# Optimization experiments

Hardware: AMD Instinct MI355X
Metric: run time of the kernel (lower is better)

## Reference

```python
import jax, jax.numpy as jnp
import numpy as np

N, K, H, HEADS, DE, MULT = 8000, 32, 256, 8, 128, 2
DH = H // HEADS
BIG_NEG = -1e9


def _ln(x, g, b):
    mu = x.mean(-1, keepdims=True)
    var = ((x - mu) ** 2).mean(-1, keepdims=True)
    return (x - mu) * jax.lax.rsqrt(var + 1e-5) * g + b


def setup_inputs() -> dict:
    key = jax.random.key(0)
    ks = iter(jax.random.split(key, 64))
    def w(shape, s=0.05):
        return (jax.random.normal(next(ks), shape, jnp.float32) * s)
    stdv = float(np.sqrt(6.0 / (HEADS + DH)))
    inp = {
        'node_features': jax.random.normal(next(ks), (N, H), jnp.float32),
        'edge_features': jax.random.normal(next(ks), (N, K, H), jnp.float32),
        'edge_attr_raw': jax.random.normal(next(ks), (N, K, DE), jnp.float32),
        'angle_embedding': jax.random.normal(next(ks), (N, HEADS, K, K), jnp.float32) * 0.1,
        'ln1n_g': jnp.ones((H,)), 'ln1n_b': jnp.zeros((H,)),
        'ln1e_g': jnp.ones((H,)), 'ln1e_b': jnp.zeros((H,)),
        'W_ea': w((DE, H)), 'b_ea': jnp.zeros((H,)),
        'W_nh': w((H, H)), 'b_nh': jnp.zeros((H,)),
        'W_eh': w((H, H)), 'b_eh': jnp.zeros((H,)),
        'W_gate': w((2 * H, H)), 'b_gate': jnp.zeros((H,)),
        'W_cand': w((2 * H, H)), 'b_cand': jnp.zeros((H,)),
        'attn_scalar': jnp.ones((HEADS,)),
        'W_in': w((H, 3 * H)), 'b_in': jnp.zeros((3 * H,)),
        'W_out': w((H, H)), 'b_out': jnp.zeros((H,)),
        'attn_weight': jax.random.uniform(next(ks), (HEADS, DH), jnp.float32, -stdv, stdv),
        'ln2n_g': jnp.ones((H,)), 'ln2n_b': jnp.zeros((H,)),
        'ln2e_g': jnp.ones((H,)), 'ln2e_b': jnp.zeros((H,)),
        'Wn1': w((H, MULT * H)), 'bn1': jnp.zeros((MULT * H,)),
        'Wn2': w((MULT * H, H)), 'bn2': jnp.zeros((H,)),
        'We1': w((H, MULT * H)), 'be1': jnp.zeros((MULT * H,)),
        'We2': w((MULT * H, H)), 'be2': jnp.zeros((H,)),
        'neighbor_list': jax.random.randint(next(ks), (N, K), 0, N),
        'neighbor_counts': jax.random.randint(next(ks), (N,), 1, K + 1),
    }
    return inp


def _forward(node_features, edge_features, edge_attr_raw, angle_embedding,
             ln1n_g, ln1n_b, ln1e_g, ln1e_b,
             W_ea, b_ea, W_nh, b_nh, W_eh, b_eh,
             W_gate, b_gate, W_cand, b_cand,
             attn_scalar, W_in, b_in, W_out, b_out, attn_weight,
             ln2n_g, ln2n_b, ln2e_g, ln2e_b,
             Wn1, bn1, Wn2, bn2, We1, be1, We2, be2,
             neighbor_list, neighbor_counts):
    mask = jnp.arange(K)[None, :] < neighbor_counts[:, None]  # [N,K] valid neighbors
    # norm_attn
    nh = _ln(node_features, ln1n_g, ln1n_b)
    eh = _ln(edge_features, ln1e_g, ln1e_b)
    # message construction
    edge_attr = jax.nn.gelu(edge_attr_raw @ W_ea + b_ea)            # [N,K,H]
    nbr = nh[neighbor_list]                                          # gather [N,K,H]
    node_hidden = jax.nn.gelu(nbr @ W_nh + b_nh)
    edge_hidden = jax.nn.gelu(eh @ W_eh + b_eh)
    m = jnp.concatenate([edge_attr, node_hidden], axis=-1)          # [N,K,2H]
    gate = jax.nn.sigmoid(m @ W_gate + b_gate)
    cand = jnp.tanh(m @ W_cand + b_cand)
    message = gate * cand + (1.0 - gate) * edge_hidden              # [N,K,H]
    # additive mask: key padding + per-head scaled angle embedding
    attn_mask = jnp.where(mask[:, None, None, :], 0.0, BIG_NEG) \
        + angle_embedding * attn_scalar[None, :, None, None]        # [N,heads,K,K]
    # multi-head self attention over the neighbor dimension
    qkv = message @ W_in + b_in                                     # [N,K,3H]
    q, k, v = jnp.split(qkv, 3, axis=-1)
    q = q.reshape(N, K, HEADS, DH)
    k = k.reshape(N, K, HEADS, DH)
    v = v.reshape(N, K, HEADS, DH)
    scores = jnp.einsum('nqhd,nkhd->nhqk', q, k) / np.float32(np.sqrt(DH)) + attn_mask
    probs = jax.nn.softmax(scores, axis=-1)
    ctx = jnp.einsum('nhqk,nkhd->nqhd', probs, v).reshape(N, K, H)
    edge_output = ctx @ W_out + b_out                               # [N,K,H]
    # graph-attention aggregation to nodes
    eo = edge_output.reshape(N, K, HEADS, DH)
    alpha = (eo * attn_weight[None, None]).sum(-1)                  # [N,K,heads]
    alpha = jax.nn.leaky_relu(alpha, 0.2)
    alpha = jnp.where(mask[:, :, None], alpha, BIG_NEG)
    alpha = jax.nn.softmax(alpha, axis=1)
    node_output = (alpha[..., None] * eo).sum(1).reshape(N, H)
    # residual + FFN
    node_f = node_output + node_features
    edge_f = edge_output + edge_features
    nh2 = _ln(node_f, ln2n_g, ln2n_b)
    eh2 = _ln(edge_f, ln2e_g, ln2e_b)
    node_f = node_f + (jax.nn.gelu(nh2 @ Wn1 + bn1) @ Wn2 + bn2)
    edge_f = edge_f + (jax.nn.gelu(eh2 @ We1 + be1) @ We2 + be2)
    return node_f, edge_f


def reference(node_features, edge_features, edge_attr_raw, angle_embedding,
              ln1n_g, ln1n_b, ln1e_g, ln1e_b,
              W_ea, b_ea, W_nh, b_nh, W_eh, b_eh,
              W_gate, b_gate, W_cand, b_cand,
              attn_scalar, W_in, b_in, W_out, b_out, attn_weight,
              ln2n_g, ln2n_b, ln2e_g, ln2e_b,
              Wn1, bn1, Wn2, bn2, We1, be1, We2, be2,
              neighbor_list, neighbor_counts):
    return _forward(node_features, edge_features, edge_attr_raw, angle_embedding,
                    ln1n_g, ln1n_b, ln1e_g, ln1e_b,
                    W_ea, b_ea, W_nh, b_nh, W_eh, b_eh,
                    W_gate, b_gate, W_cand, b_cand,
                    attn_scalar, W_in, b_in, W_out, b_out, attn_weight,
                    ln2n_g, ln2n_b, ln2e_g, ln2e_b,
                    Wn1, bn1, Wn2, bn2, We1, be1, We2, be2,
                    neighbor_list, neighbor_counts)
```

## Files before the change

### kernel.cpp

```cpp
#include <hip/hip_runtime.h>
#include <math.h>

#define NN 8000
#define KK 32
#define HH 256
#define DE 128
#define NODES 4
#define THREADS 512
#define BIGLD 536
#define LDS_BYTES (128 * BIGLD * 2)

typedef __attribute__((ext_vector_type(8))) short bs8;
typedef __attribute__((ext_vector_type(4))) short bs4;
typedef __attribute__((ext_vector_type(4))) float f4;

#define LGK_FENCE() do { asm volatile("s_waitcnt lgkmcnt(0)" ::: "memory"); __builtin_amdgcn_sched_barrier(0); } while (0)

struct P {
  const float *nf, *ef, *ear, *ang;
  const float *ln1e_g, *ln1e_b;
  const float *b_ea, *b_nh, *b_eh, *b_gate, *b_cand;
  const float *ascal, *b_in, *b_out, *aw;
  const float *ln2n_g, *ln2n_b, *ln2e_g, *ln2e_b;
  const float *bn1, *bn2, *be1, *be2;
  const int *nbrl, *nbrc;
  const unsigned short *nhb;
  const unsigned short *wtEA, *wtNH, *wtEH, *wtG, *wtC, *wtIN, *wtOUT, *wtN1, *wtN2, *wtE1, *wtE2;
  float *on, *oe;
};

__device__ __forceinline__ unsigned short f2b(float f) {
  unsigned int u = __float_as_uint(f);
  unsigned int r = (u + 0x7fffu + ((u >> 16) & 1u)) >> 16;
  return (unsigned short)r;
}
__device__ __forceinline__ float b2f(unsigned short u) {
  return __uint_as_float(((unsigned int)u) << 16);
}
__device__ __forceinline__ unsigned int cvt_pk_bf16(float lo, float hi) {
  unsigned int r;
  asm("v_cvt_pk_bf16_f32 %0, %1, %2" : "=v"(r) : "v"(lo), "v"(hi));
  return r;
}
__device__ __forceinline__ bs4 pack4(float a, float b, float c, float d) {
  union { unsigned int u[2]; bs4 v; } x;
  x.u[0] = cvt_pk_bf16(a, b);
  x.u[1] = cvt_pk_bf16(c, d);
  return x.v;
}
__device__ __forceinline__ float fast_tanh(float x) {
  x = fminf(fmaxf(x, -12.f), 12.f);
  float e = __expf(2.f * x);
  return (e - 1.f) / (e + 1.f);
}
__device__ __forceinline__ float gelu_f(float x) {
  return 0.5f * x * (1.f + fast_tanh(0.7978845608f * (x + 0.044715f * x * x * x)));
}
__device__ __forceinline__ float sigmoid_f(float x) {
  return 1.f / (1.f + __expf(-x));
}

template<int RT, int NCT, int KB, int KW>
__device__ __forceinline__ void gemmB(f4 acc[RT][NCT],
    const unsigned short* __restrict__ wt,
    const unsigned short* __restrict__ A, int cs, int l)
{
  const int lm = l & 15;
  const int lg = (l >> 4) << 3;
  #pragma unroll
  for (int kb = 0; kb < KB; ++kb) {
    bs8 wfr[NCT];
    #pragma unroll
    for (int ct = 0; ct < NCT; ++ct)
      wfr[ct] = *(const bs8*)(wt + (size_t)(cs + ct * 16 + lm) * KW + kb * 32 + lg);
    bs8 afr[RT];
    #pragma unroll
    for (int rt = 0; rt < RT; ++rt)
      afr[rt] = *(const bs8*)(A + (rt * 16 + lm) * BIGLD + kb * 32 + lg);
    #pragma unroll
    for (int rt = 0; rt < RT; ++rt)
      #pragma unroll
      for (int ct = 0; ct < NCT; ++ct)
        acc[rt][ct] = __builtin_amdgcn_mfma_f32_16x16x32_bf16(wfr[ct], afr[rt], acc[rt][ct], 0, 0, 0);
  }
}

template<int RT, int NCT>
__device__ __forceinline__ void zero_acc(f4 acc[RT][NCT]) {
  #pragma unroll
  for (int rt = 0; rt < RT; ++rt)
    #pragma unroll
    for (int ct = 0; ct < NCT; ++ct) {
      acc[rt][ct][0] = 0.f; acc[rt][ct][1] = 0.f; acc[rt][ct][2] = 0.f; acc[rt][ct][3] = 0.f;
    }
}

template<int RT, int NCT, int ACTF>
__device__ __forceinline__ void storeB(unsigned short* dst,
    f4 acc[RT][NCT], const float* __restrict__ bias, int cs, int l)
{
  const int lm = l & 15;
  const int lr = (l >> 4) << 2;
  #pragma unroll
  for (int ct = 0; ct < NCT; ++ct) {
    f4 bv = *(const f4*)(bias + cs + ct * 16 + lr);
    #pragma unroll
    for (int rt = 0; rt < RT; ++rt) {
      float v[4];
      #pragma unroll
      for (int r = 0; r < 4; ++r) {
        v[r] = acc[rt][ct][r] + bv[r];
        if (ACTF == 1) v[r] = gelu_f(v[r]);
      }
      *(bs4*)(dst + (rt * 16 + lm) * BIGLD + cs + ct * 16 + lr) = pack4(v[0], v[1], v[2], v[3]);
    }
  }
}

__global__ void node_ln_bf16(const float* __restrict__ x, const float* __restrict__ g,
                             const float* __restrict__ b, unsigned short* __restrict__ y)
{
  int row = blockIdx.x * 4 + (threadIdx.x >> 6);
  int lane = threadIdx.x & 63;
  float4 v = ((const float4*)(x + (size_t)row * HH))[lane];
  float s = v.x + v.y + v.z + v.w;
  float ss = v.x * v.x + v.y * v.y + v.z * v.z + v.w * v.w;
  #pragma unroll
  for (int m = 1; m < 64; m <<= 1) { s += __shfl_xor(s, m); ss += __shfl_xor(ss, m); }
  float mean = s * (1.f / HH);
  float var = ss * (1.f / HH) - mean * mean;
  float rstd = rsqrtf(var + 1e-5f);
  float4 gg = ((const float4*)g)[lane];
  float4 bb = ((const float4*)b)[lane];
  *(bs4*)(y + (size_t)row * HH + lane * 4) =
      pack4((v.x - mean) * rstd * gg.x + bb.x, (v.y - mean) * rstd * gg.y + bb.y,
            (v.z - mean) * rstd * gg.z + bb.z, (v.w - mean) * rstd * gg.w + bb.w);
}

__global__ void wt_transpose(const float* __restrict__ src, unsigned short* __restrict__ dst,
                             int K, int C)
{
  __shared__ float tile[32][33];
  int tx = threadIdx.x & 31, ty = threadIdx.x >> 5;
  int bk = blockIdx.x, bc = blockIdx.y;
  #pragma unroll
  for (int i = 0; i < 4; ++i)
    tile[ty + i * 8][tx] = src[(size_t)(bk * 32 + ty + i * 8) * C + bc * 32 + tx];
  __syncthreads();
  #pragma unroll
  for (int i = 0; i < 4; ++i)
    dst[(size_t)(bc * 32 + ty + i * 8) * K + bk * 32 + tx] = f2b(tile[tx][ty + i * 8]);
}

__launch_bounds__(THREADS, 2)
__global__ void mega_kernel(P p)
{
  extern __shared__ unsigned short smem[];

  const int tid = threadIdx.x;
  const int l = tid & 63;
  const int w = tid >> 6;
  const int lm = l & 15;
  const int lg = (l >> 4) << 3;
  const int lr = (l >> 4) << 2;
  const int n0 = blockIdx.x * NODES;
  const size_t ebase = (size_t)blockIdx.x * 128;
  const int4 cnt4 = *(const int4*)(p.nbrc + n0);
  const int cnts[4] = { cnt4.x, cnt4.y, cnt4.z, cnt4.w };

  #define FSA(i)  (*(float*)(smem + ((i) >> 7) * BIGLD + 256 + (((i) & 127) << 1)))
  #define FSNF(i) (*(float*)(smem + (8 + ((i) >> 7)) * BIGLD + 256 + (((i) & 127) << 1)))
  #define FLNP(j) (*(float*)(smem + 16 * BIGLD + 256 + ((j) << 1)))

  {
    int row = tid >> 2, q = tid & 3;
    const float* src = p.ear + (ebase + row) * DE + q * 32;
    unsigned short* d = smem + row * BIGLD + q * 32;
    #pragma unroll
    for (int j = 0; j < 8; ++j) {
      float4 v = ((const float4*)src)[j];
      *(bs4*)(d + j * 4) = pack4(v.x, v.y, v.z, v.w);
    }
    int idx = p.nbrl[(n0 + (row >> 5)) * KK + (row & 31)];
    const unsigned short* gsrc = p.nhb + (size_t)idx * HH + q * 64;
    unsigned short* gd = smem + row * BIGLD + 264 + q * 64;
    #pragma unroll
    for (int j = 0; j < 8; ++j) *(bs8*)(gd + j * 8) = *(const bs8*)(gsrc + j * 8);
  }
  __syncthreads();
  {
    f4 acc[8][2]; zero_acc<8,2>(acc);
    gemmB<8,2,4,128>(acc, p.wtEA, smem, w * 32, l);
    __syncthreads();
    storeB<8,2,1>(smem, acc, p.b_ea, w * 32, l);
  }
  __syncthreads();
  {
    f4 acc[8][2]; zero_acc<8,2>(acc);
    gemmB<8,2,8,256>(acc, p.wtNH, smem + 264, w * 32, l);
    __syncthreads();
    storeB<8,2,1>(smem + 256, acc, p.b_nh, w * 32, l);
  }
  __syncthreads();
  bs4 gp[8][2], cp[8][2];
  {
    f4 ga[8][2]; zero_acc<8,2>(ga);
    f4 ca[8][2]; zero_acc<8,2>(ca);
    gemmB<8,2,16,512>(ga, p.wtG, smem, w * 32, l);
    gemmB<8,2,16,512>(ca, p.wtC, smem, w * 32, l);
    #pragma unroll
    for (int ct = 0; ct < 2; ++ct) {
      f4 bg = *(const f4*)(p.b_gate + w * 32 + ct * 16 + lr);
      f4 bc = *(const f4*)(p.b_cand + w * 32 + ct * 16 + lr);
      #pragma unroll
      for (int rt = 0; rt < 8; ++rt) {
        gp[rt][ct] = pack4(sigmoid_f(ga[rt][ct][0] + bg[0]), sigmoid_f(ga[rt][ct][1] + bg[1]),
                           sigmoid_f(ga[rt][ct][2] + bg[2]), sigmoid_f(ga[rt][ct][3] + bg[3]));
        cp[rt][ct] = pack4(fast_tanh(ca[rt][ct][0] + bc[0]), fast_tanh(ca[rt][ct][1] + bc[1]),
                           fast_tanh(ca[rt][ct][2] + bc[2]), fast_tanh(ca[rt][ct][3] + bc[3]));
      }
    }
  }
  __syncthreads();
  {
    int row = tid >> 2, q = tid & 3;
    const float* src = p.ef + (ebase + row) * HH + q * 64;
    float s = 0.f, ss = 0.f;
    #pragma unroll
    for (int j = 0; j < 16; ++j) {
      float4 v = ((const float4*)src)[j];
      s += v.x + v.y + v.z + v.w;
      ss += v.x * v.x + v.y * v.y + v.z * v.z + v.w * v.w;
    }
    s += __shfl_xor(s, 1); ss += __shfl_xor(ss, 1);
    s += __shfl_xor(s, 2); ss += __shfl_xor(ss, 2);
    float mean = s * (1.f / HH);
    float var = ss * (1.f / HH) - mean * mean;
    float rstd = rsqrtf(var + 1e-5f);
    unsigned short* d = smem + row * BIGLD + q * 64;
    #pragma unroll
    for (int j = 0; j < 16; ++j) {
      float4 v = ((const float4*)src)[j];
      int c = q * 64 + j * 4;
      float4 g = *(const float4*)(p.ln1e_g + c);
      float4 b = *(const float4*)(p.ln1e_b + c);
      *(bs4*)(d + j * 4) = pack4((v.x - mean) * rstd * g.x + b.x,
                                 (v.y - mean) * rstd * g.y + b.y,
                                 (v.z - mean) * rstd * g.z + b.z,
                                 (v.w - mean) * rstd * g.w + b.w);
    }
  }
  __syncthreads();
  {
    f4 ea[8][2]; zero_acc<8,2>(ea);
    gemmB<8,2,8,256>(ea, p.wtEH, smem, w * 32, l);
    __syncthreads();
    #pragma unroll
    for (int ct = 0; ct < 2; ++ct) {
      f4 be = *(const f4*)(p.b_eh + w * 32 + ct * 16 + lr);
      #pragma unroll
      for (int rt = 0; rt < 8; ++rt) {
        float o[4];
        #pragma unroll
        for (int r = 0; r < 4; ++r) {
          float g = b2f((unsigned short)gp[rt][ct][r]);
          float c = b2f((unsigned short)cp[rt][ct][r]);
          float eh = gelu_f(ea[rt][ct][r] + be[r]);
          o[r] = g * c + (1.f - g) * eh;
        }
        *(bs4*)(smem + (rt * 16 + lm) * BIGLD + w * 32 + ct * 16 + lr) = pack4(o[0], o[1], o[2], o[3]);
      }
    }
  }
  __syncthreads();
  bs4 qp[8][2], kp[8][2], vp[8][2];
  {
    f4 acc[8][2];
    zero_acc<8,2>(acc);
    gemmB<8,2,8,256>(acc, p.wtIN, smem, w * 32, l);
    #pragma unroll
    for (int ct = 0; ct < 2; ++ct) {
      f4 bv = *(const f4*)(p.b_in + w * 32 + ct * 16 + lr);
      #pragma unroll
      for (int rt = 0; rt < 8; ++rt)
        qp[rt][ct] = pack4(acc[rt][ct][0] + bv[0], acc[rt][ct][1] + bv[1],
                           acc[rt][ct][2] + bv[2], acc[rt][ct][3] + bv[3]);
    }
    zero_acc<8,2>(acc);
    gemmB<8,2,8,256>(acc, p.wtIN + 256 * 256, smem, w * 32, l);
    #pragma unroll
    for (int ct = 0; ct < 2; ++ct) {
      f4 bv = *(const f4*)(p.b_in + 256 + w * 32 + ct * 16 + lr);
      #pragma unroll
      for (int rt = 0; rt < 8; ++rt)
        kp[rt][ct] = pack4(acc[rt][ct][0] + bv[0], acc[rt][ct][1] + bv[1],
                           acc[rt][ct][2] + bv[2], acc[rt][ct][3] + bv[3]);
    }
    zero_acc<8,2>(acc);
    gemmB<8,2,8,256>(acc, p.wtIN + 512 * 256, smem, w * 32, l);
    #pragma unroll
    for (int ct = 0; ct < 2; ++ct) {
      f4 bv = *(const f4*)(p.b_in + 512 + w * 32 + ct * 16 + lr);
      #pragma unroll
      for (int rt = 0; rt < 8; ++rt)
        vp[rt][ct] = pack4(acc[rt][ct][0] + bv[0], acc[rt][ct][1] + bv[1],
                           acc[rt][ct][2] + bv[2], acc[rt][ct][3] + bv[3]);
    }
  }
  __syncthreads();
  bs4 cxp[NODES][2][2];
  {
    const float asc = p.ascal[w];
    f4 z; z[0] = 0.f; z[1] = 0.f; z[2] = 0.f; z[3] = 0.f;
    #define WSADDR(a, r, c) ((w * 8 + (a) * 4 + ((r) >> 3)) * BIGLD + 256 + (((r) & 7) << 5) + (c))
    #pragma unroll
    for (int ni = 0; ni < NODES; ++ni) {
      #pragma unroll
      for (int j = 0; j < 2; ++j)
        #pragma unroll
        for (int ct = 0; ct < 2; ++ct) {
          *(bs4*)(smem + WSADDR(0, j * 16 + lm, ct * 16 + lr)) = qp[2 * ni + j][ct];
          *(bs4*)(smem + WSADDR(1, j * 16 + lm, ct * 16 + lr)) = kp[2 * ni + j][ct];
        }
      LGK_FENCE();
      bs8 qf[2], kf[2];
      #pragma unroll
      for (int t = 0; t < 2; ++t) {
        qf[t] = *(const bs8*)(smem + WSADDR(0, t * 16 + lm, lg));
        kf[t] = *(const bs8*)(smem + WSADDR(1, t * 16 + lm, lg));
      }
      f4 sc[2][2];
      #pragma unroll
      for (int kt = 0; kt < 2; ++kt)
        #pragma unroll
        for (int qt = 0; qt < 2; ++qt)
          sc[kt][qt] = __builtin_amdgcn_mfma_f32_16x16x32_bf16(kf[kt], qf[qt], z, 0, 0, 0);
      float inv[2];
      #pragma unroll
      for (int qt = 0; qt < 2; ++qt) {
        const int q = qt * 16 + lm;
        float sv[2][4];
        #pragma unroll
        for (int kt = 0; kt < 2; ++kt) {
          f4 av = *(const f4*)(p.ang + ((((size_t)(n0 + ni)) * 8 + w) * 32 + q) * 32 + kt * 16 + lr);
          #pragma unroll
          for (int r = 0; r < 4; ++r) {
            int kidx = kt * 16 + lr + r;
            sv[kt][r] = sc[kt][qt][r] * 0.17677669529663687f + av[r] * asc
                      + (kidx < cnts[ni] ? 0.f : -1e9f);
          }
        }
        float m = sv[0][0];
        #pragma unroll
        for (int r = 1; r < 4; ++r) m = fmaxf(m, sv[0][r]);
        #pragma unroll
        for (int r = 0; r < 4; ++r) m = fmaxf(m, sv[1][r]);
        m = fmaxf(m, __shfl_xor(m, 16));
        m = fmaxf(m, __shfl_xor(m, 32));
        float e[2][4], sum = 0.f;
        #pragma unroll
        for (int kt = 0; kt < 2; ++kt)
          #pragma unroll
          for (int r = 0; r < 4; ++r) { e[kt][r] = __expf(sv[kt][r] - m); sum += e[kt][r]; }
        sum += __shfl_xor(sum, 16);
        sum += __shfl_xor(sum, 32);
        inv[qt] = 1.f / sum;
        *(bs4*)(smem + WSADDR(0, q, lr))      = pack4(e[0][0], e[0][1], e[0][2], e[0][3]);
        *(bs4*)(smem + WSADDR(0, q, 16 + lr)) = pack4(e[1][0], e[1][1], e[1][2], e[1][3]);
      }
      #pragma unroll
      for (int j = 0; j < 2; ++j)
        #pragma unroll
        for (int ct = 0; ct < 2; ++ct)
          #pragma unroll
          for (int r = 0; r < 4; ++r)
            smem[WSADDR(1, ct * 16 + lr + r, j * 16 + lm)] = (unsigned short)vp[2 * ni + j][ct][r];
      LGK_FENCE();
      bs8 pf[2], vf[2];
      #pragma unroll
      for (int t = 0; t < 2; ++t) {
        pf[t] = *(const bs8*)(smem + WSADDR(0, t * 16 + lm, lg));
        vf[t] = *(const bs8*)(smem + WSADDR(1, t * 16 + lm, lg));
      }
      #pragma unroll
      for (int qt = 0; qt < 2; ++qt)
        #pragma unroll
        for (int dt = 0; dt < 2; ++dt) {
          f4 cx = __builtin_amdgcn_mfma_f32_16x16x32_bf16(vf[dt], pf[qt], z, 0, 0, 0);
          cxp[ni][qt][dt] = pack4(cx[0] * inv[qt], cx[1] * inv[qt], cx[2] * inv[qt], cx[3] * inv[qt]);
        }
    }
    #undef WSADDR
  }
  __syncthreads();
  {
    #pragma unroll
    for (int ni = 0; ni < NODES; ++ni)
      #pragma unroll
      for (int qt = 0; qt < 2; ++qt)
        #pragma unroll
        for (int dt = 0; dt < 2; ++dt)
          *(bs4*)(smem + (ni * 32 + qt * 16 + lm) * BIGLD + 256 + w * 32 + dt * 16 + lr) = cxp[ni][qt][dt];
  }
  __syncthreads();
  {
    f4 acc[8][2]; zero_acc<8,2>(acc);
    gemmB<8,2,8,256>(acc, p.wtOUT, smem + 256, w * 32, l);
    storeB<8,2,0>(smem, acc, p.b_out, w * 32, l);
  }
  __syncthreads();
  {
    #pragma unroll
    for (int it = 0; it < 2; ++it) {
      int idx = tid + it * 512;
      int ni = idx >> 8, rem = idx & 255;
      int k = rem >> 3, h = rem & 7;
      float aa = 0.f;
      #pragma unroll
      for (int j = 0; j < 8; ++j) {
        bs4 ev = *(const bs4*)(smem + (ni * 32 + k) * BIGLD + h * 32 + j * 4);
        float4 av = *(const float4*)(p.aw + h * 32 + j * 4);
        aa += b2f((unsigned short)ev[0]) * av.x + b2f((unsigned short)ev[1]) * av.y
            + b2f((unsigned short)ev[2]) * av.z + b2f((unsigned short)ev[3]) * av.w;
      }
      aa = aa > 0.f ? aa : 0.2f * aa;
      if (k >= cnts[ni]) aa = -1e9f;
      FSA(idx) = aa;
    }
  }
  __syncthreads();
  {
    int ni = tid >> 7, h = (tid >> 4) & 7, l16 = tid & 15;
    float v0 = FSA(ni * 256 + l16 * 8 + h);
    float v1 = FSA(ni * 256 + (l16 + 16) * 8 + h);
    float m = fmaxf(v0, v1);
    m = fmaxf(m, __shfl_xor(m, 1));
    m = fmaxf(m, __shfl_xor(m, 2));
    m = fmaxf(m, __shfl_xor(m, 4));
    m = fmaxf(m, __shfl_xor(m, 8));
    float e0 = __expf(v0 - m), e1 = __expf(v1 - m);
    float s = e0 + e1;
    s += __shfl_xor(s, 1);
    s += __shfl_xor(s, 2);
    s += __shfl_xor(s, 4);
    s += __shfl_xor(s, 8);
    float inv = 1.f / s;
    FSA(ni * 256 + l16 * 8 + h) = e0 * inv;
    FSA(ni * 256 + (l16 + 16) * 8 + h) = e1 * inv;
  }
  __syncthreads();
  float ndf[2];
  {
    #pragma unroll
    for (int it = 0; it < 2; ++it) {
      int idx = it * 512 + tid;
      int ni = idx >> 8, c = idx & 255, h = c >> 5;
      float no = 0.f;
      #pragma unroll
      for (int k = 0; k < 32; ++k)
        no = fmaf(FSA(ni * 256 + k * 8 + h), b2f(smem[(ni * 32 + k) * BIGLD + c]), no);
      float nodef = no + p.nf[(size_t)(n0 + ni) * HH + c];
      ndf[it] = nodef;
      FSNF(idx) = nodef;
      float s = nodef, ss = nodef * nodef;
      #pragma unroll
      for (int m = 1; m < 64; m <<= 1) { s += __shfl_xor(s, m); ss += __shfl_xor(ss, m); }
      if (l == 0) { FLNP(it * 8 + w) = s; FLNP(16 + it * 8 + w) = ss; }
    }
  }
  __syncthreads();
  {
    #pragma unroll
    for (int it = 0; it < 2; ++it) {
      int idx = it * 512 + tid;
      int ni = idx >> 8, c = idx & 255;
      int base = it * 8 + (ni & 1) * 4;
      float S  = FLNP(base) + FLNP(base + 1) + FLNP(base + 2) + FLNP(base + 3);
      float SS = FLNP(16 + base) + FLNP(16 + base + 1) + FLNP(16 + base + 2) + FLNP(16 + base + 3);
      float mean = S * (1.f / HH), var = SS * (1.f / HH) - mean * mean;
      float rstd = rsqrtf(var + 1e-5f);
      smem[(17 + ni) * BIGLD + 256 + c] = f2b((ndf[it] - mean) * rstd * p.ln2n_g[c] + p.ln2n_b[c]);
    }
    #pragma unroll
    for (int z = 0; z < 3; ++z) {
      int zi = z * 512 + tid;
      int zr = 21 + (zi >> 7), zc = (zi & 127) << 1;
      *(unsigned int*)(smem + zr * BIGLD + 256 + zc) = 0u;
    }
  }
  __syncthreads();
  {
    f4 acc[4];
    #pragma unroll
    for (int ct = 0; ct < 4; ++ct) { acc[ct][0]=0.f; acc[ct][1]=0.f; acc[ct][2]=0.f; acc[ct][3]=0.f; }
    #pragma unroll
    for (int kb = 0; kb < 8; ++kb) {
      bs8 afr = *(const bs8*)(smem + (17 + lm) * BIGLD + 256 + kb * 32 + lg);
      #pragma unroll
      for (int ct = 0; ct < 4; ++ct) {
        bs8 wfr = *(const bs8*)(p.wtN1 + (size_t)(w * 64 + ct * 16 + lm) * 256 + kb * 32 + lg);
        acc[ct] = __builtin_amdgcn_mfma_f32_16x16x32_bf16(wfr, afr, acc[ct], 0, 0, 0);
      }
    }
    #pragma unroll
    for (int ct = 0; ct < 4; ++ct) {
      int col = w * 64 + ct * 16 + lr;
      f4 bv = *(const f4*)(p.bn1 + col);
      *(bs4*)(smem + (33 + 2 * lm + (col >= 256 ? 1 : 0)) * BIGLD + 256 + (col & 255)) =
          pack4(gelu_f(acc[ct][0] + bv[0]), gelu_f(acc[ct][1] + bv[1]),
                gelu_f(acc[ct][2] + bv[2]), gelu_f(acc[ct][3] + bv[3]));
    }
  }
  __syncthreads();
  bs4 efp[8][2];
  {
    f4 acc[2];
    #pragma unroll
    for (int ct = 0; ct < 2; ++ct) { acc[ct][0]=0.f; acc[ct][1]=0.f; acc[ct][2]=0.f; acc[ct][3]=0.f; }
    #pragma unroll
    for (int kb = 0; kb < 16; ++kb) {
      bs8 afr = *(const bs8*)(smem + (33 + 2 * lm + (kb >> 3)) * BIGLD + 256 + (kb & 7) * 32 + lg);
      #pragma unroll
      for (int ct = 0; ct < 2; ++ct) {
        bs8 wfr = *(const bs8*)(p.wtN2 + (size_t)(w * 32 + ct * 16 + lm) * 512 + kb * 32 + lg);
        acc[ct] = __builtin_amdgcn_mfma_f32_16x16x32_bf16(wfr, afr, acc[ct], 0, 0, 0);
      }
    }
    if (lm < 4) {
      #pragma unroll
      for (int ct = 0; ct < 2; ++ct) {
        int col = w * 32 + ct * 16 + lr;
        f4 bv = *(const f4*)(p.bn2 + col);
        float4 o;
        o.x = acc[ct][0] + bv[0] + FSNF(lm * 256 + col);
        o.y = acc[ct][1] + bv[1] + FSNF(lm * 256 + col + 1);
        o.z = acc[ct][2] + bv[2] + FSNF(lm * 256 + col + 2);
        o.w = acc[ct][3] + bv[3] + FSNF(lm * 256 + col + 3);
        *(float4*)(p.on + (size_t)(n0 + lm) * HH + col) = o;
      }
    }
    #pragma unroll
    for (int rt = 0; rt < 8; ++rt)
      #pragma unroll
      for (int ct = 0; ct < 2; ++ct) {
        int row = rt * 16 + lm, col = w * 32 + ct * 16 + lr;
        bs4 ov = *(const bs4*)(smem + row * BIGLD + col);
        float4 e = *(const float4*)(p.ef + (ebase + row) * HH + col);
        efp[rt][ct] = pack4(e.x + b2f((unsigned short)ov[0]), e.y + b2f((unsigned short)ov[1]),
                            e.z + b2f((unsigned short)ov[2]), e.w + b2f((unsigned short)ov[3]));
      }
  }
  __syncthreads();
  {
    int row = tid >> 2, q = tid & 3;
    const float* efs = p.ef + (ebase + row) * HH + q * 64;
    const unsigned short* eor = smem + row * BIGLD + q * 64;
    float xv[64];
    float s = 0.f, ss = 0.f;
    #pragma unroll
    for (int j = 0; j < 16; ++j) {
      float4 e = ((const float4*)efs)[j];
      bs4 ov = *(const bs4*)(eor + j * 4);
      float x0 = e.x + b2f((unsigned short)ov[0]);
      float x1 = e.y + b2f((unsigned short)ov[1]);
      float x2 = e.z + b2f((unsigned short)ov[2]);
      float x3 = e.w + b2f((unsigned short)ov[3]);
      xv[j * 4] = x0; xv[j * 4 + 1] = x1; xv[j * 4 + 2] = x2; xv[j * 4 + 3] = x3;
      s += x0 + x1 + x2 + x3;
      ss += x0 * x0 + x1 * x1 + x2 * x2 + x3 * x3;
    }
    s += __shfl_xor(s, 1); ss += __shfl_xor(ss, 1);
    s += __shfl_xor(s, 2); ss += __shfl_xor(ss, 2);
    float mean = s * (1.f / HH);
    float var = ss * (1.f / HH) - mean * mean;
    float rstd = rsqrtf(var + 1e-5f);
    unsigned short* d = smem + row * BIGLD + q * 64;
    #pragma unroll
    for (int j = 0; j < 16; ++j) {
      int c = q * 64 + j * 4;
      float4 g = *(const float4*)(p.ln2e_g + c);
      float4 b = *(const float4*)(p.ln2e_b + c);
      *(bs4*)(d + j * 4) = pack4((xv[j * 4] - mean) * rstd * g.x + b.x,
                                 (xv[j * 4 + 1] - mean) * rstd * g.y + b.y,
                                 (xv[j * 4 + 2] - mean) * rstd * g.z + b.z,
                                 (xv[j * 4 + 3] - mean) * rstd * g.w + b.w);
    }
  }
  __syncthreads();
  f4 oacc[8][2]; zero_acc<8,2>(oacc);
  {
    f4 h[8][2]; zero_acc<8,2>(h);
    gemmB<8,2,8,256>(h, p.wtE1, smem, w * 32, l);
    storeB<8,2,1>(smem + 256, h, p.be1, w * 32, l);
  }
  __syncthreads();
  {
    gemmB<8,2,8,512>(oacc, p.wtE2, smem + 256, w * 32, l);
    f4 h[8][2]; zero_acc<8,2>(h);
    gemmB<8,2,8,256>(h, p.wtE1 + (size_t)256 * 256, smem, w * 32, l);
    __syncthreads();
    storeB<8,2,1>(smem + 256, h, p.be1 + 256, w * 32, l);
  }
  __syncthreads();
  {
    gemmB<8,2,8,512>(oacc, p.wtE2 + 256, smem + 256, w * 32, l);
    #pragma unroll
    for (int ct = 0; ct < 2; ++ct) {
      f4 bv = *(const f4*)(p.be2 + w * 32 + ct * 16 + lr);
      #pragma unroll
      for (int rt = 0; rt < 8; ++rt) {
        int row = rt * 16 + lm;
        float4 o;
        o.x = oacc[rt][ct][0] + bv[0] + b2f((unsigned short)efp[rt][ct][0]);
        o.y = oacc[rt][ct][1] + bv[1] + b2f((unsigned short)efp[rt][ct][1]);
        o.z = oacc[rt][ct][2] + bv[2] + b2f((unsigned short)efp[rt][ct][2]);
        o.w = oacc[rt][ct][3] + bv[3] + b2f((unsigned short)efp[rt][ct][3]);
        *(float4*)(p.oe + (ebase + row) * HH + w * 32 + ct * 16 + lr) = o;
      }
    }
  }
  #undef FSA
  #undef FSNF
  #undef FLNP
}

extern "C" void kernel_launch(void* const* d_in, const int* in_sizes, int n_in,
                              void* d_out, int out_size, void* d_ws, size_t ws_size,
                              hipStream_t stream)
{
  P p;
  p.nf     = (const float*)d_in[0];
  p.ef     = (const float*)d_in[1];
  p.ear    = (const float*)d_in[2];
  p.ang    = (const float*)d_in[3];
  const float* ln1n_g = (const float*)d_in[4];
  const float* ln1n_b = (const float*)d_in[5];
  p.ln1e_g = (const float*)d_in[6];  p.ln1e_b = (const float*)d_in[7];
  const float* W_ea   = (const float*)d_in[8];  p.b_ea   = (const float*)d_in[9];
  const float* W_nh   = (const float*)d_in[10]; p.b_nh   = (const float*)d_in[11];
  const float* W_eh   = (const float*)d_in[12]; p.b_eh   = (const float*)d_in[13];
  const float* W_gate = (const float*)d_in[14]; p.b_gate = (const float*)d_in[15];
  const float* W_cand = (const float*)d_in[16]; p.b_cand = (const float*)d_in[17];
  p.ascal  = (const float*)d_in[18];
  const float* W_in   = (const float*)d_in[19]; p.b_in   = (const float*)d_in[20];
  const float* W_out  = (const float*)d_in[21]; p.b_out  = (const float*)d_in[22];
  p.aw     = (const float*)d_in[23];
  p.ln2n_g = (const float*)d_in[24]; p.ln2n_b = (const float*)d_in[25];
  p.ln2e_g = (const float*)d_in[26]; p.ln2e_b = (const float*)d_in[27];
  const float* Wn1 = (const float*)d_in[28]; p.bn1 = (const float*)d_in[29];
  const float* Wn2 = (const float*)d_in[30]; p.bn2 = (const float*)d_in[31];
  const float* We1 = (const float*)d_in[32]; p.be1 = (const float*)d_in[33];
  const float* We2 = (const float*)d_in[34]; p.be2 = (const float*)d_in[35];
  p.nbrl   = (const int*)d_in[36];
  p.nbrc   = (const int*)d_in[37];
  p.on     = (float*)d_out;
  p.oe     = (float*)d_out + (size_t)NN * HH;

  size_t off = 0;
  auto alloc = [&](size_t elems) {
    unsigned short* q = (unsigned short*)((char*)d_ws + off);
    off += elems * 2;
    return q;
  };
  unsigned short* nhb = alloc((size_t)NN * HH);
  unsigned short* wtEA  = alloc(256 * 128);
  unsigned short* wtNH  = alloc(256 * 256);
  unsigned short* wtEH  = alloc(256 * 256);
  unsigned short* wtG   = alloc(256 * 512);
  unsigned short* wtC   = alloc(256 * 512);
  unsigned short* wtIN  = alloc(768 * 256);
  unsigned short* wtOUT = alloc(256 * 256);
  unsigned short* wtN1  = alloc(512 * 256);
  unsigned short* wtN2  = alloc(256 * 512);
  unsigned short* wtE1  = alloc(512 * 256);
  unsigned short* wtE2  = alloc(256 * 512);
  p.nhb = nhb;
  p.wtEA = wtEA; p.wtNH = wtNH; p.wtEH = wtEH; p.wtG = wtG; p.wtC = wtC;
  p.wtIN = wtIN; p.wtOUT = wtOUT; p.wtN1 = wtN1; p.wtN2 = wtN2; p.wtE1 = wtE1; p.wtE2 = wtE2;

  node_ln_bf16<<<NN / 4, 256, 0, stream>>>((const float*)d_in[0], ln1n_g, ln1n_b, nhb);

  auto tr = [&](const float* src, unsigned short* dst, int K, int C) {
    wt_transpose<<<dim3(K / 32, C / 32), 256, 0, stream>>>(src, dst, K, C);
  };
  tr(W_ea, wtEA, 128, 256);
  tr(W_nh, wtNH, 256, 256);
  tr(W_eh, wtEH, 256, 256);
  tr(W_gate, wtG, 512, 256);
  tr(W_cand, wtC, 512, 256);
  tr(W_in, wtIN, 256, 768);
  tr(W_out, wtOUT, 256, 256);
  tr(Wn1, wtN1, 256, 512);
  tr(Wn2, wtN2, 512, 256);
  tr(We1, wtE1, 256, 512);
  tr(We2, wtE2, 512, 256);

  (void)hipFuncSetAttribute((const void*)mega_kernel,
                            hipFuncAttributeMaxDynamicSharedMemorySize, LDS_BYTES);
  mega_kernel<<<NN / NODES, THREADS, LDS_BYTES, stream>>>(p);
}
```

Before: 1.632 ms.

## Tile edge GEMMs as 2x4 warp grid of 64x64 instead of 128x32

Changes the per-warp tile for most 128-row edge GEMMs from all 128 rows by 32 columns to a 64x64 block, with warps arranged as a 2x4 grid. A row-base parameter is added to the GEMM and store helpers. Per k-step each warp now issues 8 fragment loads for 16 MFMAs instead of 10, which cuts LDS and global weight-fragment traffic. Each weight fragment is fetched by two warps instead of one, and the in-projection GEMM keeps the old layout.

```diff
diff --git a/kernel.cpp b/kernel.cpp
--- a/kernel.cpp
+++ b/kernel.cpp
@@ -63,7 +63,7 @@
 template<int RT, int NCT, int KB, int KW>
 __device__ __forceinline__ void gemmB(f4 acc[RT][NCT],
     const unsigned short* __restrict__ wt,
-    const unsigned short* __restrict__ A, int cs, int l)
+    const unsigned short* __restrict__ A, int cs, int rb, int l)
 {
   const int lm = l & 15;
   const int lg = (l >> 4) << 3;
@@ -76,7 +76,7 @@
     bs8 afr[RT];
     #pragma unroll
     for (int rt = 0; rt < RT; ++rt)
-      afr[rt] = *(const bs8*)(A + (rt * 16 + lm) * BIGLD + kb * 32 + lg);
+      afr[rt] = *(const bs8*)(A + (rb + rt * 16 + lm) * BIGLD + kb * 32 + lg);
     #pragma unroll
     for (int rt = 0; rt < RT; ++rt)
       #pragma unroll
@@ -97,7 +97,7 @@
 
 template<int RT, int NCT, int ACTF>
 __device__ __forceinline__ void storeB(unsigned short* dst,
-    f4 acc[RT][NCT], const float* __restrict__ bias, int cs, int l)
+    f4 acc[RT][NCT], const float* __restrict__ bias, int cs, int rb, int l)
 {
   const int lm = l & 15;
   const int lr = (l >> 4) << 2;
@@ -112,7 +112,7 @@
         v[r] = acc[rt][ct][r] + bv[r];
         if (ACTF == 1) v[r] = gelu_f(v[r]);
       }
-      *(bs4*)(dst + (rt * 16 + lm) * BIGLD + cs + ct * 16 + lr) = pack4(v[0], v[1], v[2], v[3]);
+      *(bs4*)(dst + (rb + rt * 16 + lm) * BIGLD + cs + ct * 16 + lr) = pack4(v[0], v[1], v[2], v[3]);
     }
   }
 }
@@ -163,6 +163,8 @@
   const int lm = l & 15;
   const int lg = (l >> 4) << 3;
   const int lr = (l >> 4) << 2;
+  const int w2r = (w >> 2) * 64;
+  const int w2c = (w & 3) * 64;
   const int n0 = blockIdx.x * NODES;
   const size_t ebase = (size_t)blockIdx.x * 128;
   const int4 cnt4 = *(const int4*)(p.nbrc + n0);
@@ -189,31 +191,31 @@
   }
   __syncthreads();
   {
-    f4 acc[8][2]; zero_acc<8,2>(acc);
-    gemmB<8,2,4,128>(acc, p.wtEA, smem, w * 32, l);
+    f4 acc[4][4]; zero_acc<4,4>(acc);
+    gemmB<4,4,4,128>(acc, p.wtEA, smem, w2c, w2r, l);
     __syncthreads();
-    storeB<8,2,1>(smem, acc, p.b_ea, w * 32, l);
-  }
-  __syncthreads();
-  {
-    f4 acc[8][2]; zero_acc<8,2>(acc);
-    gemmB<8,2,8,256>(acc, p.wtNH, smem + 264, w * 32, l);
+    storeB<4,4,1>(smem, acc, p.b_ea, w2c, w2r, l);
+  }
+  __syncthreads();
+  {
+    f4 acc[4][4]; zero_acc<4,4>(acc);
+    gemmB<4,4,8,256>(acc, p.wtNH, smem + 264, w2c, w2r, l);
     __syncthreads();
-    storeB<8,2,1>(smem + 256, acc, p.b_nh, w * 32, l);
-  }
-  __syncthreads();
-  bs4 gp[8][2], cp[8][2];
-  {
-    f4 ga[8][2]; zero_acc<8,2>(ga);
-    f4 ca[8][2]; zero_acc<8,2>(ca);
-    gemmB<8,2,16,512>(ga, p.wtG, smem, w * 32, l);
-    gemmB<8,2,16,512>(ca, p.wtC, smem, w * 32, l);
-    #pragma unroll
-    for (int ct = 0; ct < 2; ++ct) {
-      f4 bg = *(const f4*)(p.b_gate + w * 32 + ct * 16 + lr);
-      f4 bc = *(const f4*)(p.b_cand + w * 32 + ct * 16 + lr);
-      #pragma unroll
-      for (int rt = 0; rt < 8; ++rt) {
+    storeB<4,4,1>(smem + 256, acc, p.b_nh, w2c, w2r, l);
+  }
+  __syncthreads();
+  bs4 gp[4][4], cp[4][4];
+  {
+    f4 ga[4][4]; zero_acc<4,4>(ga);
+    f4 ca[4][4]; zero_acc<4,4>(ca);
+    gemmB<4,4,16,512>(ga, p.wtG, smem, w2c, w2r, l);
+    gemmB<4,4,16,512>(ca, p.wtC, smem, w2c, w2r, l);
+    #pragma unroll
+    for (int ct = 0; ct < 4; ++ct) {
+      f4 bg = *(const f4*)(p.b_gate + w2c + ct * 16 + lr);
+      f4 bc = *(const f4*)(p.b_cand + w2c + ct * 16 + lr);
+      #pragma unroll
+      for (int rt = 0; rt < 4; ++rt) {
         gp[rt][ct] = pack4(sigmoid_f(ga[rt][ct][0] + bg[0]), sigmoid_f(ga[rt][ct][1] + bg[1]),
                            sigmoid_f(ga[rt][ct][2] + bg[2]), sigmoid_f(ga[rt][ct][3] + bg[3]));
         cp[rt][ct] = pack4(fast_tanh(ca[rt][ct][0] + bc[0]), fast_tanh(ca[rt][ct][1] + bc[1]),
@@ -252,14 +254,14 @@
   }
   __syncthreads();
   {
-    f4 ea[8][2]; zero_acc<8,2>(ea);
-    gemmB<8,2,8,256>(ea, p.wtEH, smem, w * 32, l);
+    f4 ea[4][4]; zero_acc<4,4>(ea);
+    gemmB<4,4,8,256>(ea, p.wtEH, smem, w2c, w2r, l);
     __syncthreads();
     #pragma unroll
-    for (int ct = 0; ct < 2; ++ct) {
-      f4 be = *(const f4*)(p.b_eh + w * 32 + ct * 16 + lr);
-      #pragma unroll
-      for (int rt = 0; rt < 8; ++rt) {
+    for (int ct = 0; ct < 4; ++ct) {
+      f4 be = *(const f4*)(p.b_eh + w2c + ct * 16 + lr);
+      #pragma unroll
+      for (int rt = 0; rt < 4; ++rt) {
         float o[4];
         #pragma unroll
         for (int r = 0; r < 4; ++r) {
@@ -268,7 +270,7 @@
           float eh = gelu_f(ea[rt][ct][r] + be[r]);
           o[r] = g * c + (1.f - g) * eh;
         }
-        *(bs4*)(smem + (rt * 16 + lm) * BIGLD + w * 32 + ct * 16 + lr) = pack4(o[0], o[1], o[2], o[3]);
+        *(bs4*)(smem + (w2r + rt * 16 + lm) * BIGLD + w2c + ct * 16 + lr) = pack4(o[0], o[1], o[2], o[3]);
       }
     }
   }
@@ -277,7 +279,7 @@
   {
     f4 acc[8][2];
     zero_acc<8,2>(acc);
-    gemmB<8,2,8,256>(acc, p.wtIN, smem, w * 32, l);
+    gemmB<8,2,8,256>(acc, p.wtIN, smem, w * 32, 0, l);
     #pragma unroll
     for (int ct = 0; ct < 2; ++ct) {
       f4 bv = *(const f4*)(p.b_in + w * 32 + ct * 16 + lr);
@@ -287,7 +289,7 @@
                            acc[rt][ct][2] + bv[2], acc[rt][ct][3] + bv[3]);
     }
     zero_acc<8,2>(acc);
-    gemmB<8,2,8,256>(acc, p.wtIN + 256 * 256, smem, w * 32, l);
+    gemmB<8,2,8,256>(acc, p.wtIN + 256 * 256, smem, w * 32, 0, l);
     #pragma unroll
     for (int ct = 0; ct < 2; ++ct) {
       f4 bv = *(const f4*)(p.b_in + 256 + w * 32 + ct * 16 + lr);
@@ -297,7 +299,7 @@
                            acc[rt][ct][2] + bv[2], acc[rt][ct][3] + bv[3]);
     }
     zero_acc<8,2>(acc);
-    gemmB<8,2,8,256>(acc, p.wtIN + 512 * 256, smem, w * 32, l);
+    gemmB<8,2,8,256>(acc, p.wtIN + 512 * 256, smem, w * 32, 0, l);
     #pragma unroll
     for (int ct = 0; ct < 2; ++ct) {
       f4 bv = *(const f4*)(p.b_in + 512 + w * 32 + ct * 16 + lr);
@@ -404,9 +406,9 @@
   }
   __syncthreads();
   {
-    f4 acc[8][2]; zero_acc<8,2>(acc);
-    gemmB<8,2,8,256>(acc, p.wtOUT, smem + 256, w * 32, l);
-    storeB<8,2,0>(smem, acc, p.b_out, w * 32, l);
+    f4 acc[4][4]; zero_acc<4,4>(acc);
+    gemmB<4,4,8,256>(acc, p.wtOUT, smem + 256, w2c, w2r, l);
+    storeB<4,4,0>(smem, acc, p.b_out, w2c, w2r, l);
   }
   __syncthreads();
   {
@@ -512,7 +514,7 @@
     }
   }
   __syncthreads();
-  bs4 efp[8][2];
+  bs4 efp[4][4];
   {
     f4 acc[2];
     #pragma unroll
@@ -540,10 +542,10 @@
       }
     }
     #pragma unroll
-    for (int rt = 0; rt < 8; ++rt)
-      #pragma unroll
-      for (int ct = 0; ct < 2; ++ct) {
-        int row = rt * 16 + lm, col = w * 32 + ct * 16 + lr;
+    for (int rt = 0; rt < 4; ++rt)
+      #pragma unroll
+      for (int ct = 0; ct < 4; ++ct) {
+        int row = w2r + rt * 16 + lm, col = w2c + ct * 16 + lr;
         bs4 ov = *(const bs4*)(smem + row * BIGLD + col);
         float4 e = *(const float4*)(p.ef + (ebase + row) * HH + col);
         efp[rt][ct] = pack4(e.x + b2f((unsigned short)ov[0]), e.y + b2f((unsigned short)ov[1]),
@@ -587,35 +589,35 @@
     }
   }
   __syncthreads();
-  f4 oacc[8][2]; zero_acc<8,2>(oacc);
-  {
-    f4 h[8][2]; zero_acc<8,2>(h);
-    gemmB<8,2,8,256>(h, p.wtE1, smem, w * 32, l);
-    storeB<8,2,1>(smem + 256, h, p.be1, w * 32, l);
-  }
-  __syncthreads();
-  {
-    gemmB<8,2,8,512>(oacc, p.wtE2, smem + 256, w * 32, l);
-    f4 h[8][2]; zero_acc<8,2>(h);
-    gemmB<8,2,8,256>(h, p.wtE1 + (size_t)256 * 256, smem, w * 32, l);
+  f4 oacc[4][4]; zero_acc<4,4>(oacc);
+  {
+    f4 h[4][4]; zero_acc<4,4>(h);
+    gemmB<4,4,8,256>(h, p.wtE1, smem, w2c, w2r, l);
+    storeB<4,4,1>(smem + 256, h, p.be1, w2c, w2r, l);
+  }
+  __syncthreads();
+  {
+    gemmB<4,4,8,512>(oacc, p.wtE2, smem + 256, w2c, w2r, l);
+    f4 h[4][4]; zero_acc<4,4>(h);
+    gemmB<4,4,8,256>(h, p.wtE1 + (size_t)256 * 256, smem, w2c, w2r, l);
     __syncthreads();
-    storeB<8,2,1>(smem + 256, h, p.be1 + 256, w * 32, l);
-  }
-  __syncthreads();
-  {
-    gemmB<8,2,8,512>(oacc, p.wtE2 + 256, smem + 256, w * 32, l);
-    #pragma unroll
-    for (int ct = 0; ct < 2; ++ct) {
-      f4 bv = *(const f4*)(p.be2 + w * 32 + ct * 16 + lr);
-      #pragma unroll
-      for (int rt = 0; rt < 8; ++rt) {
-        int row = rt * 16 + lm;
+    storeB<4,4,1>(smem + 256, h, p.be1 + 256, w2c, w2r, l);
+  }
+  __syncthreads();
+  {
+    gemmB<4,4,8,512>(oacc, p.wtE2 + 256, smem + 256, w2c, w2r, l);
+    #pragma unroll
+    for (int ct = 0; ct < 4; ++ct) {
+      f4 bv = *(const f4*)(p.be2 + w2c + ct * 16 + lr);
+      #pragma unroll
+      for (int rt = 0; rt < 4; ++rt) {
+        int row = w2r + rt * 16 + lm;
         float4 o;
         o.x = oacc[rt][ct][0] + bv[0] + b2f((unsigned short)efp[rt][ct][0]);
         o.y = oacc[rt][ct][1] + bv[1] + b2f((unsigned short)efp[rt][ct][1]);
         o.z = oacc[rt][ct][2] + bv[2] + b2f((unsigned short)efp[rt][ct][2]);
         o.w = oacc[rt][ct][3] + bv[3] + b2f((unsigned short)efp[rt][ct][3]);
-        *(float4*)(p.oe + (ebase + row) * HH + w * 32 + ct * 16 + lr) = o;
+        *(float4*)(p.oe + (ebase + row) * HH + w2c + ct * 16 + lr) = o;
       }
     }
   }
```

Result: slower. 1.978 ms (+21.1%).
